# Kernel tuning notes

Hardware: AMD Instinct MI355X
Metric: run time of the kernel (lower is better)

The kernel has to match this reference:

```python
import jax, jax.numpy as jnp
import numpy as np

H, D = 16, 64  # n_heads, head_dim


def l2norm(t):
    # F.normalize(t, p=2, dim=-1)
    return t / jnp.maximum(jnp.linalg.norm(t, axis=-1, keepdims=True), 1e-12)


def setup_inputs() -> dict:
    key = jax.random.key(0)
    ks = jax.random.split(key, 6)
    B, N, C = 2, 2048, 1024
    x = jax.random.normal(ks[0], (B, N, C), jnp.float32)
    pos_bias = jax.random.normal(ks[1], (1, H, N, N), jnp.float32)
    mask = jnp.zeros((B, 1, 1, N), bool)  # attn_mask: True = masked
    Wqkv = jax.random.normal(ks[2], (C, 3 * H * D), jnp.float32) / np.sqrt(C)
    Wout = jax.random.normal(ks[3], (H * D, C), jnp.float32) / np.sqrt(H * D)
    Wpre = jax.random.normal(ks[4], (H, H), jnp.float32) / np.sqrt(H)   # 1x1 conv pre
    bpre = jnp.zeros((H,), jnp.float32)
    Wpost = jax.random.normal(ks[5], (H, H), jnp.float32) / np.sqrt(H)  # 1x1 conv post
    bpost = jnp.zeros((H,), jnp.float32)
    temperature = jnp.float32(15.5)
    return {"x": x, "pos_bias": pos_bias, "mask": mask, "Wqkv": Wqkv,
            "Wout": Wout, "Wpre": Wpre, "bpre": bpre, "Wpost": Wpost,
            "bpost": bpost, "temperature": temperature}


def reference(x, pos_bias, mask, Wqkv, Wout, Wpre, bpre, Wpost, bpost, temperature):
    B, N, C = x.shape
    # qkv: 'b n (h d qkv) -> qkv b h n d'
    qkv = (x @ Wqkv).reshape(B, N, H, D, 3)
    q = jnp.transpose(qkv[..., 0], (0, 2, 1, 3))  # [B,H,N,D]
    k = jnp.transpose(qkv[..., 1], (0, 2, 1, 3))
    v = jnp.transpose(qkv[..., 2], (0, 2, 1, 3))
    q, k = l2norm(q), l2norm(k)  # cosine_sim
    kv = jnp.stack([k, v], axis=0)  # attach_cache with cache=None
    # temperature-scaled cosine-sim scores
    dots = jnp.einsum('bhid,bhjd->bhij', q, k) * temperature
    # talking heads pre (1x1 conv over head channel)
    dots = jnp.einsum('gh,bhij->bgij', Wpre, dots) + bpre[None, :, None, None]
    dots = dots + pos_bias
    dots = jnp.where(mask, -jnp.finfo(dots.dtype).max, dots)
    attn = jax.nn.softmax(dots, axis=-1)
    # talking heads post
    attn = jnp.einsum('gh,bhij->bgij', Wpost, attn) + bpost[None, :, None, None]
    out = jnp.einsum('bhij,bhjd->bhid', attn, v)  # [B,H,N,D]
    out = jnp.transpose(out, (0, 2, 1, 3)).reshape(B, N, H * D) @ Wout
    return (out, kv)
```

## Files before the change

### kernel.cpp

```cpp
#include <hip/hip_runtime.h>
#include <stdint.h>

typedef __attribute__((ext_vector_type(8))) short bf16x8;
typedef __attribute__((ext_vector_type(4))) float f32x4;
typedef __attribute__((ext_vector_type(4))) short short4v;

#define DEV __device__ __forceinline__
#define L2E 1.4426950408889634f

DEV float bf2f(unsigned short s){ union{unsigned int u; float f;} x; x.u = ((unsigned int)s)<<16; return x.f; }
DEV unsigned short f2bf(float f){ union{float f; unsigned int u;} x; x.f = f; x.u += 0x7fffu + ((x.u>>16)&1u); return (unsigned short)(x.u>>16); }

DEV f32x4 mfma16(bf16x8 a, bf16x8 b, f32x4 c){
  return __builtin_amdgcn_mfma_f32_16x16x32_bf16(a, b, c, 0, 0, 0);
}
DEV f32x4 zero4(){ f32x4 z; z[0]=0.f; z[1]=0.f; z[2]=0.f; z[3]=0.f; return z; }
DEV bf16x8 zerob(){ bf16x8 z; z[0]=0;z[1]=0;z[2]=0;z[3]=0;z[4]=0;z[5]=0;z[6]=0;z[7]=0; return z; }
DEV float fexp2(float x){ float r; asm volatile("v_exp_f32 %0, %1" : "=v"(r) : "v"(x)); return r; }
DEV void barw(){ asm volatile("s_waitcnt lgkmcnt(0)" ::: "memory"); __builtin_amdgcn_s_barrier(); }

__global__ __launch_bounds__(256) void k_f32_to_bf16(const float* __restrict__ in, unsigned short* __restrict__ out, int n4){
  int i = blockIdx.x*256 + threadIdx.x;
  if (i < n4){
    float4 v = ((const float4*)in)[i];
    short4v o; o.x=(short)f2bf(v.x); o.y=(short)f2bf(v.y); o.z=(short)f2bf(v.z); o.w=(short)f2bf(v.w);
    ((short4v*)out)[i] = o;
  }
}

__global__ __launch_bounds__(256) void k_convT(const float* __restrict__ in, unsigned short* __restrict__ out, int R, int Cc){
  __shared__ float t[32][33];
  int c0 = blockIdx.x*32, r0 = blockIdx.y*32;
  int tid = threadIdx.x;
  int row = tid>>3, col4 = (tid&7)*4;
  float4 v = *(const float4*)&in[(size_t)(r0+row)*Cc + c0 + col4];
  t[row][col4+0]=v.x; t[row][col4+1]=v.y; t[row][col4+2]=v.z; t[row][col4+3]=v.w;
  __syncthreads();
  short4v o;
  o.x=(short)f2bf(t[col4+0][row]); o.y=(short)f2bf(t[col4+1][row]);
  o.z=(short)f2bf(t[col4+2][row]); o.w=(short)f2bf(t[col4+3][row]);
  *(short4v*)&out[(size_t)(c0+row)*R + r0 + col4] = o;
}

__global__ __launch_bounds__(256) void k_prep(const float* __restrict__ wpre, const float* __restrict__ wpost,
                                              const float* __restrict__ temp,
                                              unsigned short* __restrict__ wpre_t,
                                              unsigned short* __restrict__ wpre_t2,
                                              unsigned short* __restrict__ wpost_b){
  int t = threadIdx.x;
  float T = temp[0];
  wpre_t[t]  = f2bf(wpre[t]*T);
  wpre_t2[t] = f2bf(wpre[t]*T*L2E);
  wpost_b[t] = f2bf(wpost[t]);
}

__global__ __launch_bounds__(256) void k_maskf(const unsigned char* __restrict__ mask, float* __restrict__ maskf){
  int i = blockIdx.x*256 + threadIdx.x;
  if (i < 4096) maskf[i] = mask[i] ? -1e30f : 0.f;
}

template<int OUTF>
__global__ __launch_bounds__(256,2) void k_gemm(const unsigned short* __restrict__ A, const unsigned short* __restrict__ Bt,
                                                void* __restrict__ Cv, int M, int Nn, int K){
  __shared__ unsigned short As[128][72];
  __shared__ unsigned short Bs[128][72];
  int tid = threadIdx.x;
  int n0 = blockIdx.x*128, m0 = blockIdx.y*128;
  int w = tid>>6, lane = tid&63, lg = lane>>4, lp = lane&15;
  int wm = (w>>1)*64, wn = (w&1)*64;
  f32x4 acc[4][4];
  #pragma unroll
  for (int i=0;i<4;++i)
    #pragma unroll
    for (int j=0;j<4;++j) acc[i][j] = zero4();

  for (int kt=0; kt<K; kt+=64){
    #pragma unroll
    for (int cch=0; cch<4; ++cch){
      int e = tid + cch*256; int r = e>>3, cl = (e&7)*8;
      *(bf16x8*)&As[r][cl] = *(const bf16x8*)&A[(size_t)(m0+r)*K + kt + cl];
      *(bf16x8*)&Bs[r][cl] = *(const bf16x8*)&Bt[(size_t)(n0+r)*K + kt + cl];
    }
    __syncthreads();
    #pragma unroll
    for (int ks=0; ks<2; ++ks){
      bf16x8 a[4], b[4];
      #pragma unroll
      for (int mi=0; mi<4; ++mi) a[mi] = *(const bf16x8*)&As[wm+mi*16+lp][ks*32 + lg*8];
      #pragma unroll
      for (int ni=0; ni<4; ++ni) b[ni] = *(const bf16x8*)&Bs[wn+ni*16+lp][ks*32 + lg*8];
      #pragma unroll
      for (int mi=0; mi<4; ++mi)
        #pragma unroll
        for (int ni=0; ni<4; ++ni)
          acc[mi][ni] = mfma16(a[mi], b[ni], acc[mi][ni]);
    }
    __syncthreads();
  }
  #pragma unroll
  for (int mi=0; mi<4; ++mi)
    #pragma unroll
    for (int ni=0; ni<4; ++ni)
      #pragma unroll
      for (int r=0; r<4; ++r){
        int row = m0+wm+mi*16+lg*4+r, col = n0+wn+ni*16+lp;
        if (OUTF) ((float*)Cv)[(size_t)row*Nn+col] = acc[mi][ni][r];
        else ((unsigned short*)Cv)[(size_t)row*Nn+col] = f2bf(acc[mi][ni][r]);
      }
}

__global__ __launch_bounds__(256) void k_split_norm(const unsigned short* __restrict__ qkv,
                                                    unsigned short* __restrict__ q, unsigned short* __restrict__ k,
                                                    unsigned short* __restrict__ v, float* __restrict__ kv_out){
  int w = threadIdx.x>>6, lane = threadIdx.x&63;
  int widx = blockIdx.x*4 + w;
  int h = widx & 15; int bn = widx >> 4;
  int b = bn >> 11; int n = bn & 2047;
  size_t base = (size_t)bn*3072 + h*192 + lane*3;
  float qv = bf2f(qkv[base]), kvv = bf2f(qkv[base+1]), vv = bf2f(qkv[base+2]);
  float nq = qv*qv, nk = kvv*kvv;
  #pragma unroll
  for (int m=1; m<64; m<<=1){ nq += __shfl_xor(nq, m); nk += __shfl_xor(nk, m); }
  float qn = qv / fmaxf(sqrtf(nq), 1e-12f);
  float kn = kvv / fmaxf(sqrtf(nk), 1e-12f);
  size_t idx = ((size_t)(b*16+h)*2048 + n)*64 + lane;
  q[idx] = f2bf(qn); k[idx] = f2bf(kn); v[idx] = f2bf(vv);
  kv_out[idx] = kn;
  kv_out[4194304 + idx] = vv;
}

__global__ __launch_bounds__(256) void k_transpose_v(const unsigned short* __restrict__ v, unsigned short* __restrict__ vt){
  __shared__ unsigned short t[64][72];
  int bh = blockIdx.y; int n0 = blockIdx.x*64;
  int tid = threadIdx.x;
  #pragma unroll
  for (int cch=0; cch<2; ++cch){
    int e = tid + cch*256; int r = e>>3, c8 = (e&7)*8;
    *(bf16x8*)&t[r][c8] = *(const bf16x8*)&v[((size_t)bh*2048 + n0 + r)*64 + c8];
  }
  __syncthreads();
  #pragma unroll
  for (int cch=0; cch<2; ++cch){
    int e = tid + cch*256; int d = e>>3, nn8 = (e&7)*8;
    bf16x8 o;
    #pragma unroll
    for (int i=0;i<8;++i) o[i] = (short)t[nn8+i][d];
    *(bf16x8*)&vt[((size_t)bh*64 + d)*2048 + n0 + nn8] = o;
  }
}

__global__ __launch_bounds__(256) void k_vsum(const unsigned short* __restrict__ v, float* __restrict__ vsum){
  int bg = blockIdx.x;
  int d = threadIdx.x & 63, part = threadIdx.x>>6;
  float s = 0.f;
  for (int n = part*512; n < part*512+512; ++n) s += bf2f(v[((size_t)bg*2048 + n)*64 + d]);
  __shared__ float red[4][64];
  red[part][d] = s; __syncthreads();
  if (part==0) vsum[bg*64 + d] = red[0][d]+red[1][d]+red[2][d]+red[3][d];
}

__global__ __launch_bounds__(512,4) void k_score(
    const unsigned short* __restrict__ q,
    const unsigned short* __restrict__ kk,
    const float* __restrict__ pos_bias,
    const float* __restrict__ maskf,
    const unsigned short* __restrict__ wpre_t2,
    const float* __restrict__ bpre,
    unsigned short* __restrict__ Pb,
    float* __restrict__ part_l)
{
  __shared__ __align__(16) char smem[40960];
  const int tid = threadIdx.x;
  const int w = tid>>6, lane = tid&63, lg = lane>>4, lp = lane&15;
  const int bid = blockIdx.x;
  const int qd = bid>>4, r2 = bid&15;
  const int b = r2>>3, n = qd*8 + (r2&7);
  const int it = n>>2, js = n&3;
  const int i0 = it*16, jsb = js*512;

  bf16x8 qf[2][2];
  #pragma unroll
  for (int hh=0; hh<2; ++hh){
    const unsigned short* qb = q + ((size_t)(b*16+2*w+hh)*2048 + i0 + lp)*64;
    qf[hh][0] = *(const bf16x8*)(qb + lg*8);
    qf[hh][1] = *(const bf16x8*)(qb + 32 + lg*8);
  }
  bf16x8 preA = zerob();
  if (lg < 2) preA = *(const bf16x8*)&wpre_t2[lp*16 + lg*8];
  float bpre_s[4];
  #pragma unroll
  for (int r=0;r<4;++r) bpre_s[r] = bpre[lg*4+r]*L2E - 32.0f;

  float sacc[2][4];
  #pragma unroll
  for (int ii=0;ii<2;++ii)
    #pragma unroll
    for (int r=0;r<4;++r) sacc[ii][r] = 0.f;

  const size_t kbase0 = (size_t)(b*16 + 2*w)*131072;
  const size_t kbase1 = (size_t)(b*16 + 2*w+1)*131072;

  bf16x8 k0v[4], k1v[4];
  #pragma unroll
  for (int kf=0; kf<2; ++kf)
    #pragma unroll
    for (int jf=0; jf<2; ++jf){
      size_t off = (size_t)(jsb + jf*16 + lp)*64 + kf*32 + lg*8;
      k0v[kf*2+jf] = *(const bf16x8*)(kk + kbase0 + off);
      k1v[kf*2+jf] = *(const bf16x8*)(kk + kbase1 + off);
    }

  for (int t=0; t<16; ++t){
    const int j0 = jsb + t*32;
    const int j0n = jsb + ((t+1)&15)*32;
    char* sbuf = smem + (t&1)*20480;
    float pbt[4][4];
    #pragma unroll
    for (int cc=0; cc<4; ++cc){
      int il = 2*w + (cc>>1);
      int jl = (cc&1)*16 + lp;
      #pragma unroll
      for (int r=0;r<4;++r)
        pbt[cc][r] = pos_bias[(size_t)(lg*4+r)*4194304 + (size_t)(i0+il)*2048 + j0 + jl];
    }
    float mk0 = maskf[b*2048 + j0 + lp];
    float mk1 = maskf[b*2048 + j0 + 16 + lp];

    f32x4 s0[2], s1[2];
    #pragma unroll
    for (int jf=0;jf<2;++jf){ s0[jf]=zero4(); s1[jf]=zero4(); }
    #pragma unroll
    for (int kf=0; kf<2; ++kf)
      #pragma unroll
      for (int jf=0; jf<2; ++jf){
        s0[jf] = mfma16(qf[0][kf], k0v[kf*2+jf], s0[jf]);
        s1[jf] = mfma16(qf[1][kf], k1v[kf*2+jf], s1[jf]);
      }
    #pragma unroll
    for (int jf=0;jf<2;++jf)
      #pragma unroll
      for (int r=0;r<4;++r){
        int ij = (lg*4+r)*32 + jf*16 + lp;
        unsigned int pk = (unsigned int)f2bf(s0[jf][r]) | ((unsigned int)f2bf(s1[jf][r])<<16);
        *(unsigned int*)(sbuf + ij*40 + w*4) = pk;
      }
    #pragma unroll
    for (int kf=0; kf<2; ++kf)
      #pragma unroll
      for (int jf=0; jf<2; ++jf){
        size_t off = (size_t)(j0n + jf*16 + lp)*64 + kf*32 + lg*8;
        k0v[kf*2+jf] = *(const bf16x8*)(kk + kbase0 + off);
        k1v[kf*2+jf] = *(const bf16x8*)(kk + kbase1 + off);
      }
    barw();

    #pragma unroll
    for (int cc=0; cc<4; ++cc){
      int c = w*4+cc;
      int il = 2*w + (cc>>1);
      int jl = (cc&1)*16 + lp;
      bf16x8 sfrag = zerob();
      if (lg < 2) sfrag = *(const bf16x8*)(sbuf + (c*16+lp)*40 + lg*16);
      f32x4 pa = mfma16(preA, sfrag, zero4());
      float mkj = (cc&1) ? mk1 : mk0;
      float pv0 = fexp2(fmaf(pbt[cc][0], L2E, pa[0] + bpre_s[0] + mkj));
      float pv1 = fexp2(fmaf(pbt[cc][1], L2E, pa[1] + bpre_s[1] + mkj));
      float pv2 = fexp2(fmaf(pbt[cc][2], L2E, pa[2] + bpre_s[2] + mkj));
      float pv3 = fexp2(fmaf(pbt[cc][3], L2E, pa[3] + bpre_s[3] + mkj));
      sacc[cc>>1][0] += pv0; sacc[cc>>1][1] += pv1;
      sacc[cc>>1][2] += pv2; sacc[cc>>1][3] += pv3;
      short4v p4;
      p4.x = (short)f2bf(pv0); p4.y = (short)f2bf(pv1);
      p4.z = (short)f2bf(pv2); p4.w = (short)f2bf(pv3);
      *(short4v*)&Pb[(((size_t)(b*2048 + i0+il)*2048) + j0 + jl)*16 + lg*4] = p4;
    }
  }

  #pragma unroll
  for (int ii=0;ii<2;++ii)
    #pragma unroll
    for (int r=0;r<4;++r){
      float v = sacc[ii][r];
      #pragma unroll
      for (int m=1; m<16; m<<=1) v += __shfl_xor(v, m);
      sacc[ii][r] = v;
    }
  if (lp == 0){
    int base = ((b*128+it)*4 + js)*256;
    #pragma unroll
    for (int ii=0;ii<2;++ii){
      float4 st; st.x = sacc[ii][0]; st.y = sacc[ii][1]; st.z = sacc[ii][2]; st.w = sacc[ii][3];
      *(float4*)&part_l[base + (2*w+ii)*16 + lg*4] = st;
    }
  }
}

__global__ __launch_bounds__(512,4) void k_mix(
    const unsigned short* __restrict__ Pb,
    const unsigned short* __restrict__ vt,
    const unsigned short* __restrict__ wpost_b,
    const float* __restrict__ bpost,
    const float* __restrict__ vsum,
    const float* __restrict__ part_l,
    float* __restrict__ pout0,
    float* __restrict__ pout1)
{
  __shared__ __align__(16) char smem[33792];
  float* linv = (float*)(smem + 32768);
  const int tid = threadIdx.x;
  const int w = tid>>6, lane = tid&63, lg = lane>>4, lp = lane&15;
  const int bid = blockIdx.x;
  const int qd = bid>>4, r2 = bid&15;
  const int b = r2>>3, n = qd*8 + (r2&7);
  const int it = n>>1, js = n&1;
  const int i0 = it*16, jsb = js*1024;

  if (tid < 256){
    int base = ((b*128+it)*4)*256 + tid;
    float sum = part_l[base] + part_l[base+256] + part_l[base+512] + part_l[base+768];
    linv[tid] = 1.f/sum;
  }
  __syncthreads();

  bf16x8 postB[2];
  #pragma unroll
  for (int ii=0;ii<2;++ii){
    postB[ii] = zerob();
    if (lg < 2){
      bf16x8 wf = *(const bf16x8*)&wpost_b[lp*16 + lg*8];
      int i = 2*w+ii;
      #pragma unroll
      for (int e=0;e<8;++e){
        float vsc = bf2f((unsigned short)wf[e]) * linv[i*16 + lg*8 + e];
        postB[ii][e] = (short)f2bf(vsc);
      }
    }
  }

  f32x4 oacc[2][4];
  #pragma unroll
  for (int hh=0; hh<2; ++hh)
    #pragma unroll
    for (int df=0; df<4; ++df) oacc[hh][df] = zero4();

  __syncthreads();

  for (int t=0; t<32; ++t){
    const int j0 = jsb + t*32;
    char* abuf = smem + (t&1)*16384;
    bf16x8 pfr[4];
    #pragma unroll
    for (int cc=0; cc<4; ++cc){
      int il = 2*w + (cc>>1);
      pfr[cc] = zerob();
      if (lg < 2)
        pfr[cc] = *(const bf16x8*)&Pb[(((size_t)(b*2048 + i0+il)*2048) + j0 + (cc&1)*16 + lp)*16 + lg*8];
    }
    bf16x8 vfr[2][4];
    #pragma unroll
    for (int hh=0; hh<2; ++hh)
      #pragma unroll
      for (int df=0; df<4; ++df)
        vfr[hh][df] = *(const bf16x8*)(vt + ((size_t)(b*16+2*w+hh)*64 + df*16 + lp)*2048 + j0 + lg*8);
    #pragma unroll
    for (int cc=0; cc<4; ++cc){
      int il = 2*w + (cc>>1);
      f32x4 aa = mfma16(pfr[cc], postB[cc>>1], zero4());
      short4v av;
      av.x = (short)f2bf(aa[0]); av.y = (short)f2bf(aa[1]);
      av.z = (short)f2bf(aa[2]); av.w = (short)f2bf(aa[3]);
      int row = lp*16 + il;
      int chunk = ((cc&1)*4 + lg) ^ ((lp ^ il)&6);
      *(short4v*)(abuf + row*64 + chunk*8) = av;
    }
    barw();
    #pragma unroll
    for (int hh=0; hh<2; ++hh){
      int gg = 2*w+hh;
      bf16x8 af = *(const bf16x8*)(abuf + (gg*16+lp)*64 + (((lg*2) ^ ((gg^lp)&6))*8));
      #pragma unroll
      for (int df=0; df<4; ++df)
        oacc[hh][df] = mfma16(af, vfr[hh][df], oacc[hh][df]);
    }
  }

  float* po = js ? pout1 : pout0;
  #pragma unroll
  for (int hh=0; hh<2; ++hh){
    int gg = 2*w+hh;
    float bp = (js==0) ? bpost[gg] : 0.f;
    #pragma unroll
    for (int df=0; df<4; ++df){
      int d = df*16+lp;
      float vs = vsum[(b*16+gg)*64 + d];
      #pragma unroll
      for (int r=0;r<4;++r){
        po[((size_t)b*2048 + i0 + lg*4 + r)*1024 + gg*64 + d] = oacc[hh][df][r] + bp*vs;
      }
    }
  }
}

__global__ __launch_bounds__(256) void k_combine(const float* __restrict__ p0, const float* __restrict__ p1,
                                                 unsigned short* __restrict__ ao){
  int i = blockIdx.x*256 + threadIdx.x;
  float4 a = ((const float4*)p0)[i];
  float4 c = ((const float4*)p1)[i];
  short4v o;
  o.x=(short)f2bf(a.x+c.x); o.y=(short)f2bf(a.y+c.y);
  o.z=(short)f2bf(a.z+c.z); o.w=(short)f2bf(a.w+c.w);
  ((short4v*)ao)[i] = o;
}

__global__ __launch_bounds__(512,6) void k_pass1f(
    const unsigned short* __restrict__ q,
    const unsigned short* __restrict__ kk,
    const float* __restrict__ pos_bias,
    const unsigned char* __restrict__ mask,
    const unsigned short* __restrict__ wpre_t,
    const float* __restrict__ bpre,
    float* __restrict__ part_m,
    float* __restrict__ part_l)
{
  __shared__ __align__(16) char smem[40960];
  const int tid = threadIdx.x;
  const int w = tid>>6, lane = tid&63, lg = lane>>4, lp = lane&15;
  const int bid = blockIdx.x;
  const int js = bid & 3, b = (bid>>2)&1, it = bid>>3;
  const int i0 = it*16, jsb = js*512;

  *(f32x4*)(smem + tid*80 + 32) = zero4();
  *(f32x4*)(smem + tid*80 + 48) = zero4();

  bf16x8 qf[2][2];
  #pragma unroll
  for (int hh=0; hh<2; ++hh){
    const unsigned short* qb = q + ((size_t)(b*16+2*w+hh)*2048 + i0 + lp)*64;
    qf[hh][0] = *(const bf16x8*)(qb + lg*8);
    qf[hh][1] = *(const bf16x8*)(qb + 32 + lg*8);
  }
  bf16x8 preB = zerob();
  if (lg < 2) preB = *(const bf16x8*)&wpre_t[lp*16 + lg*8];
  const float bpre_g = bpre[lp];

  float m[2], s[2];
  m[0] = -3.0e38f; m[1] = -3.0e38f; s[0] = 0.f; s[1] = 0.f;
  const size_t kbase0 = (size_t)(b*16 + 2*w)*131072;
  const size_t kbase1 = (size_t)(b*16 + 2*w+1)*131072;

  __syncthreads();

  for (int t=0; t<16; ++t){
    const int j0 = jsb + t*32;
    f32x4 s0[2], s1[2];
    #pragma unroll
    for (int jf=0;jf<2;++jf){ s0[jf]=zero4(); s1[jf]=zero4(); }
    #pragma unroll
    for (int kf=0; kf<2; ++kf){
      #pragma unroll
      for (int jf=0; jf<2; ++jf){
        size_t off = (size_t)(j0 + jf*16 + lp)*64 + kf*32 + lg*8;
        bf16x8 k0 = *(const bf16x8*)(kk + kbase0 + off);
        bf16x8 k1 = *(const bf16x8*)(kk + kbase1 + off);
        s0[jf] = mfma16(qf[0][kf], k0, s0[jf]);
        s1[jf] = mfma16(qf[1][kf], k1, s1[jf]);
      }
    }
    #pragma unroll
    for (int jf=0;jf<2;++jf)
      #pragma unroll
      for (int r=0;r<4;++r){
        int ij = (lg*4+r)*32 + jf*16 + lp;
        unsigned int pk = (unsigned int)f2bf(s0[jf][r]) | ((unsigned int)f2bf(s1[jf][r])<<16);
        *(unsigned int*)(smem + ij*80 + w*4) = pk;
      }
    __syncthreads();

    unsigned int mku0 = *(const unsigned int*)(mask + b*2048 + j0 + lg*4);
    unsigned int mku1 = *(const unsigned int*)(mask + b*2048 + j0 + 16 + lg*4);
    #pragma unroll
    for (int cc=0; cc<4; ++cc){
      int c = w*4+cc;
      bf16x8 afr = *(const bf16x8*)(smem + (c*16+lp)*80 + lg*16);
      f32x4 pa = mfma16(afr, preB, zero4());
      int il = 2*w + (cc>>1);
      int jl = (cc&1)*16 + lg*4;
      float4 pb = *(const float4*)&pos_bias[((size_t)lp*2048 + (i0+il))*2048 + j0 + jl];
      unsigned int mku = (cc&1) ? mku1 : mku0;
      float va0 = pa[0] + pb.x + bpre_g + (((mku    )&255u) ? -1e30f : 0.f);
      float va1 = pa[1] + pb.y + bpre_g + (((mku>> 8)&255u) ? -1e30f : 0.f);
      float va2 = pa[2] + pb.z + bpre_g + (((mku>>16)&255u) ? -1e30f : 0.f);
      float va3 = pa[3] + pb.w + bpre_g + (((mku>>24)&255u) ? -1e30f : 0.f);
      int ii = cc>>1;
      float vm = fmaxf(fmaxf(va0,va1), fmaxf(va2,va3));
      float nm = fmaxf(m[ii], vm);
      s[ii] = s[ii]*__expf(m[ii]-nm) + __expf(va0-nm)+__expf(va1-nm)+__expf(va2-nm)+__expf(va3-nm);
      m[ii] = nm;
    }
    __syncthreads();
  }

  #pragma unroll
  for (int ii=0; ii<2; ++ii){
    #pragma unroll
    for (int mk_=16; mk_<=32; mk_<<=1){
      float m2 = __shfl_xor(m[ii], mk_);
      float l2 = __shfl_xor(s[ii], mk_);
      float nm = fmaxf(m[ii], m2);
      s[ii] = s[ii]*__expf(m[ii]-nm) + l2*__expf(m2-nm);
      m[ii] = nm;
    }
  }
  if (lg == 0){
    int pidx = ((b*128+it)*4 + js)*256;
    #pragma unroll
    for (int ii=0; ii<2; ++ii){
      part_m[pidx + (2*w+ii)*16 + lp] = m[ii];
      part_l[pidx + (2*w+ii)*16 + lp] = s[ii];
    }
  }
}

__global__ __launch_bounds__(512,4) void k_pass2f(
    const unsigned short* __restrict__ q,
    const unsigned short* __restrict__ kk,
    const unsigned short* __restrict__ vt,
    const float* __restrict__ pos_bias,
    const unsigned char* __restrict__ mask,
    const unsigned short* __restrict__ wpre_t,
    const unsigned short* __restrict__ wpost_b,
    const float* __restrict__ bpre,
    const float* __restrict__ bpost,
    const float* __restrict__ vsum,
    const float* __restrict__ part_m,
    const float* __restrict__ part_l,
    float* __restrict__ pout0,
    float* __restrict__ pout1)
{
  __shared__ __align__(16) char smem[61440];
  const int tid = threadIdx.x;
  const int w = tid>>6, lane = tid&63, lg = lane>>4, lp = lane&15;
  const int bid = blockIdx.x;
  const int js = bid & 1, b = (bid>>1)&1, it = bid>>2;
  const int i0 = it*16, jsb = js*1024;

  *(f32x4*)(smem + tid*80 + 32) = zero4();
  *(f32x4*)(smem + tid*80 + 48) = zero4();

  bf16x8 qf[2][2];
  #pragma unroll
  for (int hh=0; hh<2; ++hh){
    const unsigned short* qb = q + ((size_t)(b*16+2*w+hh)*2048 + i0 + lp)*64;
    qf[hh][0] = *(const bf16x8*)(qb + lg*8);
    qf[hh][1] = *(const bf16x8*)(qb + 32 + lg*8);
  }
  bf16x8 preB = zerob(), postB = zerob();
  if (lg < 2){
    preB  = *(const bf16x8*)&wpre_t[lp*16 + lg*8];
    postB = *(const bf16x8*)&wpost_b[lp*16 + lg*8];
  }
  const float bpre_g = bpre[lp];

  float mC[2], linvC[2];
  {
    float lC[2]; mC[0]=mC[1]=-3.0e38f; lC[0]=lC[1]=0.f;
    int base = ((b*128+it)*4)*256;
    #pragma unroll
    for (int sj=0; sj<4; ++sj){
      #pragma unroll
      for (int ii=0; ii<2; ++ii){
        float mp  = part_m[base + sj*256 + (2*w+ii)*16 + lp];
        float lpv = part_l[base + sj*256 + (2*w+ii)*16 + lp];
        float nm = fmaxf(mC[ii], mp);
        lC[ii] = lC[ii]*__expf(mC[ii]-nm) + lpv*__expf(mp-nm);
        mC[ii] = nm;
      }
    }
    linvC[0] = 1.f/lC[0]; linvC[1] = 1.f/lC[1];
  }

  f32x4 oacc[2][4];
  #pragma unroll
  for (int hh=0; hh<2; ++hh)
    #pragma unroll
    for (int df=0; df<4; ++df) oacc[hh][df] = zero4();

  const size_t kbase0 = (size_t)(b*16 + 2*w)*131072;
  const size_t kbase1 = (size_t)(b*16 + 2*w+1)*131072;

  __syncthreads();

  for (int t=0; t<32; ++t){
    const int j0 = jsb + t*32;
    f32x4 s0[2], s1[2];
    #pragma unroll
    for (int jf=0;jf<2;++jf){ s0[jf]=zero4(); s1[jf]=zero4(); }
    #pragma unroll
    for (int kf=0; kf<2; ++kf){
      #pragma unroll
      for (int jf=0; jf<2; ++jf){
        size_t off = (size_t)(j0 + jf*16 + lp)*64 + kf*32 + lg*8;
        bf16x8 k0 = *(const bf16x8*)(kk + kbase0 + off);
        bf16x8 k1 = *(const bf16x8*)(kk + kbase1 + off);
        s0[jf] = mfma16(qf[0][kf], k0, s0[jf]);
        s1[jf] = mfma16(qf[1][kf], k1, s1[jf]);
      }
    }
    #pragma unroll
    for (int jf=0;jf<2;++jf)
      #pragma unroll
      for (int r=0;r<4;++r){
        int ij = (lg*4+r)*32 + jf*16 + lp;
        unsigned int pk = (unsigned int)f2bf(s0[jf][r]) | ((unsigned int)f2bf(s1[jf][r])<<16);
        *(unsigned int*)(smem + ij*80 + w*4) = pk;
      }
    __syncthreads();

    unsigned int mku0 = *(const unsigned int*)(mask + b*2048 + j0 + lg*4);
    unsigned int mku1 = *(const unsigned int*)(mask + b*2048 + j0 + 16 + lg*4);
    #pragma unroll
    for (int cc=0; cc<4; ++cc){
      int c = w*4+cc;
      bf16x8 afr = *(const bf16x8*)(smem + (c*16+lp)*80 + lg*16);
      f32x4 pa = mfma16(afr, preB, zero4());
      int il = 2*w + (cc>>1);
      int jl = (cc&1)*16 + lg*4;
      float4 pb = *(const float4*)&pos_bias[((size_t)lp*2048 + (i0+il))*2048 + j0 + jl];
      unsigned int mku = (cc&1) ? mku1 : mku0;
      float va0 = pa[0] + pb.x + bpre_g + (((mku    )&255u) ? -1e30f : 0.f);
      float va1 = pa[1] + pb.y + bpre_g + (((mku>> 8)&255u) ? -1e30f : 0.f);
      float va2 = pa[2] + pb.z + bpre_g + (((mku>>16)&255u) ? -1e30f : 0.f);
      float va3 = pa[3] + pb.w + bpre_g + (((mku>>24)&255u) ? -1e30f : 0.f);
      int ii = cc>>1;
      int rowb = (c*16 + lg*4);
      *(unsigned short*)(smem + (rowb+0)*80 + lp*2) = f2bf(__expf(va0-mC[ii])*linvC[ii]);
      *(unsigned short*)(smem + (rowb+1)*80 + lp*2) = f2bf(__expf(va1-mC[ii])*linvC[ii]);
      *(unsigned short*)(smem + (rowb+2)*80 + lp*2) = f2bf(__expf(va2-mC[ii])*linvC[ii]);
      *(unsigned short*)(smem + (rowb+3)*80 + lp*2) = f2bf(__expf(va3-mC[ii])*linvC[ii]);
    }
    __syncthreads();

    #pragma unroll
    for (int cc=0; cc<4; ++cc){
      int c = w*4+cc;
      bf16x8 a2 = *(const bf16x8*)(smem + (c*16+lp)*80 + lg*16);
      f32x4 aa = mfma16(a2, postB, zero4());
      int il = 2*w + (cc>>1);
      int jl = (cc&1)*16 + lg*4;
      short4v av;
      av.x = (short)f2bf(aa[0]); av.y = (short)f2bf(aa[1]);
      av.z = (short)f2bf(aa[2]); av.w = (short)f2bf(aa[3]);
      *(short4v*)(smem + 40960 + (lp*16 + il)*80 + jl*2) = av;
    }
    __syncthreads();

    #pragma unroll
    for (int hh=0; hh<2; ++hh){
      int gg = 2*w+hh;
      bf16x8 af = *(const bf16x8*)(smem + 40960 + (gg*16+lp)*80 + lg*16);
      #pragma unroll
      for (int df=0; df<4; ++df){
        bf16x8 vf = *(const bf16x8*)(vt + ((size_t)(b*16+gg)*64 + df*16 + lp)*2048 + j0 + lg*8);
        oacc[hh][df] = mfma16(af, vf, oacc[hh][df]);
      }
    }
    __syncthreads();
  }

  float* po = js ? pout1 : pout0;
  #pragma unroll
  for (int hh=0; hh<2; ++hh){
    int gg = 2*w+hh;
    float bp = (js==0) ? bpost[gg] : 0.f;
    #pragma unroll
    for (int df=0; df<4; ++df){
      int d = df*16+lp;
      float vs = vsum[(b*16+gg)*64 + d];
      #pragma unroll
      for (int r=0;r<4;++r){
        po[((size_t)b*2048 + i0 + lg*4 + r)*1024 + gg*64 + d] = oacc[hh][df][r] + bp*vs;
      }
    }
  }
}

extern "C" void kernel_launch(void* const* d_in, const int* in_sizes, int n_in,
                              void* d_out, int out_size, void* d_ws, size_t ws_size,
                              hipStream_t stream)
{
  const float* x        = (const float*)d_in[0];
  const float* pos_bias = (const float*)d_in[1];
  const unsigned char* mask = (const unsigned char*)d_in[2];
  const float* Wqkv     = (const float*)d_in[3];
  const float* Wout     = (const float*)d_in[4];
  const float* Wpre     = (const float*)d_in[5];
  const float* bpre     = (const float*)d_in[6];
  const float* Wpost    = (const float*)d_in[7];
  const float* bpost    = (const float*)d_in[8];
  const float* temp     = (const float*)d_in[9];
  float* out = (float*)d_out;
  float* kv_out = out + 4194304;

  char* ws = (char*)d_ws;
  unsigned short* XB    = (unsigned short*)(ws + 0);
  unsigned short* WT    = (unsigned short*)(ws + 8388608);
  unsigned short* WOT   = (unsigned short*)(ws + 8388608);
  float*          PART_M= (float*)        (ws + 10485760);
  float*          PART_L= (float*)        (ws + 11534336);
  unsigned short* WPRE  = (unsigned short*)(ws + 12582912);
  unsigned short* WPRE2 = (unsigned short*)(ws + 12583424);
  unsigned short* WPOST = (unsigned short*)(ws + 12583936);
  float*          VSUM  = (float*)        (ws + 12584448);
  float*          MASKF = (float*)        (ws + 12593152);
  unsigned short* QKV   = (unsigned short*)(ws + 14680064);
  unsigned short* VT    = (unsigned short*)(ws + 14680064);
  float*          POUT0 = (float*)        (ws + 23068672);
  unsigned short* Q     = (unsigned short*)(ws + 39845888);
  unsigned short* KB    = (unsigned short*)(ws + 48234496);
  unsigned short* VB    = (unsigned short*)(ws + 56623104);
  float*          POUT1 = (float*)        (ws + 56623104);
  unsigned short* PB    = (unsigned short*)(ws + 75497472);
  unsigned short* AO    = XB;

  const int use_new = (ws_size >= (size_t)343932928);

  k_f32_to_bf16<<<4096, 256, 0, stream>>>(x, XB, 1048576);
  k_convT<<<dim3(96,32), 256, 0, stream>>>(Wqkv, WT, 1024, 3072);
  k_gemm<0><<<dim3(24,32), 256, 0, stream>>>(XB, WT, (void*)QKV, 4096, 3072, 1024);
  k_split_norm<<<16384, 256, 0, stream>>>(QKV, Q, KB, VB, kv_out);
  k_transpose_v<<<dim3(32,32), 256, 0, stream>>>(VB, VT);
  k_vsum<<<32, 256, 0, stream>>>(VB, VSUM);
  k_prep<<<1, 256, 0, stream>>>(Wpre, Wpost, temp, WPRE, WPRE2, WPOST);
  k_maskf<<<16, 256, 0, stream>>>(mask, MASKF);
  k_convT<<<dim3(32,32), 256, 0, stream>>>(Wout, WOT, 1024, 1024);

  if (use_new){
    k_score<<<1024, 512, 0, stream>>>(Q, KB, pos_bias, MASKF, WPRE2, bpre, PB, PART_L);
    k_mix<<<512, 512, 0, stream>>>(PB, VT, WPOST, bpost, VSUM, PART_L, POUT0, POUT1);
  } else {
    k_pass1f<<<1024, 512, 0, stream>>>(Q, KB, pos_bias, mask, WPRE, bpre, PART_M, PART_L);
    k_pass2f<<<512, 512, 0, stream>>>(Q, KB, VT, pos_bias, mask, WPRE, WPOST, bpre, bpost, VSUM,
                                      PART_M, PART_L, POUT0, POUT1);
  }
  k_combine<<<4096, 256, 0, stream>>>(POUT0, POUT1, AO);
  k_gemm<1><<<dim3(8,32), 256, 0, stream>>>(AO, WOT, d_out, 4096, 1024, 1024);
}
```

Baseline: 522.2 us.

## Precompute exp(pos_bias) in fp16 and factor it out of score softmax

Adds a kernel that converts pos_bias into exp(pos_bias) stored as fp16, packed with all 16 heads per (i,j). The score kernel then multiplies exp of the mixed score by this factor. It uses a fixed offset of -32 in place of a running max, and it prefetches K tiles and the exp-bias tiles one step ahead with double-buffered shared memory. The aim is to halve pos_bias read bytes in the hot kernel, make them contiguous, and drop max tracking. The cost is an extra pass over the full 64 MB pos_bias each call and a new 134 MB buffer. The fixed -32 offset and fp16 storage of exp(pos_bias) also raise overflow and underflow risk. The old two-pass fallback is removed.

Result: slower. 668.2 us (+28.0%).

```diff
diff --git a/kernel.cpp b/kernel.cpp
--- a/kernel.cpp
+++ b/kernel.cpp
@@ -1,4 +1,5 @@
 #include <hip/hip_runtime.h>
+#include <hip/hip_fp16.h>
 #include <stdint.h>
 
 typedef __attribute__((ext_vector_type(8))) short bf16x8;
@@ -10,6 +11,8 @@
 
 DEV float bf2f(unsigned short s){ union{unsigned int u; float f;} x; x.u = ((unsigned int)s)<<16; return x.f; }
 DEV unsigned short f2bf(float f){ union{float f; unsigned int u;} x; x.f = f; x.u += 0x7fffu + ((x.u>>16)&1u); return (unsigned short)(x.u>>16); }
+DEV float h2f(unsigned short u){ return __half2float(__ushort_as_half(u)); }
+DEV unsigned short f2h(float f){ return __half_as_ushort(__float2half(f)); }
 
 DEV f32x4 mfma16(bf16x8 a, bf16x8 b, f32x4 c){
   return __builtin_amdgcn_mfma_f32_16x16x32_bf16(a, b, c, 0, 0, 0);
@@ -44,12 +47,10 @@
 
 __global__ __launch_bounds__(256) void k_prep(const float* __restrict__ wpre, const float* __restrict__ wpost,
                                               const float* __restrict__ temp,
-                                              unsigned short* __restrict__ wpre_t,
                                               unsigned short* __restrict__ wpre_t2,
                                               unsigned short* __restrict__ wpost_b){
   int t = threadIdx.x;
   float T = temp[0];
-  wpre_t[t]  = f2bf(wpre[t]*T);
   wpre_t2[t] = f2bf(wpre[t]*T*L2E);
   wpost_b[t] = f2bf(wpost[t]);
 }
@@ -57,6 +58,23 @@
 __global__ __launch_bounds__(256) void k_maskf(const unsigned char* __restrict__ mask, float* __restrict__ maskf){
   int i = blockIdx.x*256 + threadIdx.x;
   if (i < 4096) maskf[i] = mask[i] ? -1e30f : 0.f;
+}
+
+__global__ __launch_bounds__(256) void k_pbexp(const float* __restrict__ pb, unsigned short* __restrict__ epb){
+  int idx = blockIdx.x*256 + threadIdx.x;
+  int i = idx >> 11, j = idx & 2047;
+  unsigned int pk[8];
+  #pragma unroll
+  for (int g2=0; g2<8; ++g2){
+    float a = fexp2(pb[(size_t)(2*g2  )*4194304 + (size_t)i*2048 + j] * L2E);
+    float b = fexp2(pb[(size_t)(2*g2+1)*4194304 + (size_t)i*2048 + j] * L2E);
+    pk[g2] = (unsigned int)f2h(a) | ((unsigned int)f2h(b)<<16);
+  }
+  uint4 o0, o1;
+  o0.x=pk[0]; o0.y=pk[1]; o0.z=pk[2]; o0.w=pk[3];
+  o1.x=pk[4]; o1.y=pk[5]; o1.z=pk[6]; o1.w=pk[7];
+  *(uint4*)&epb[(size_t)idx*16]     = o0;
+  *(uint4*)&epb[(size_t)idx*16 + 8] = o1;
 }
 
 template<int OUTF>
@@ -159,7 +177,208 @@
   if (part==0) vsum[bg*64 + d] = red[0][d]+red[1][d]+red[2][d]+red[3][d];
 }
 
-__global__ __launch_bounds__(512,4) void k_score(
+__global__ __launch_bounds__(512,4) void k_score2(
+    const unsigned short* __restrict__ q,
+    const unsigned short* __restrict__ kk,
+    const unsigned short* __restrict__ epb,
+    const float* __restrict__ maskf,
+    const unsigned short* __restrict__ wpre_t2,
+    const float* __restrict__ bpre,
+    unsigned short* __restrict__ Pb,
+    float* __restrict__ part_l)
+{
+  __shared__ __align__(16) char smem[40960];
+  const int tid = threadIdx.x;
+  const int w = tid>>6, lane = tid&63, lg = lane>>4, lp = lane&15;
+  const int bid = blockIdx.x;
+  const int qd = bid>>4, r2 = bid&15;
+  const int b = r2>>3, n = qd*8 + (r2&7);
+  const int it = n>>2, js = n&3;
+  const int i0 = it*16, jsb = js*512;
+  const int mbase = b*2048;
+
+  bf16x8 qf[2][2];
+  #pragma unroll
+  for (int hh=0; hh<2; ++hh){
+    const unsigned short* qb = q + ((size_t)(b*16+2*w+hh)*2048 + i0 + lp)*64;
+    qf[hh][0] = *(const bf16x8*)(qb + lg*8);
+    qf[hh][1] = *(const bf16x8*)(qb + 32 + lg*8);
+  }
+  bf16x8 preA = zerob();
+  if (lg < 2) preA = *(const bf16x8*)&wpre_t2[lp*16 + lg*8];
+  float bpre_s[4];
+  #pragma unroll
+  for (int r=0;r<4;++r) bpre_s[r] = bpre[lg*4+r]*L2E - 32.0f;
+
+  float sacc[2][4];
+  #pragma unroll
+  for (int ii=0;ii<2;++ii)
+    #pragma unroll
+    for (int r=0;r<4;++r) sacc[ii][r] = 0.f;
+
+  const size_t kbase0 = (size_t)(b*16 + 2*w)*131072;
+  const size_t kbase1 = (size_t)(b*16 + 2*w+1)*131072;
+
+  bf16x8 k0v[4], k1v[4];
+  #pragma unroll
+  for (int kf=0; kf<2; ++kf)
+    #pragma unroll
+    for (int jf=0; jf<2; ++jf){
+      size_t off = (size_t)(jsb + jf*16 + lp)*64 + kf*32 + lg*8;
+      k0v[kf*2+jf] = *(const bf16x8*)(kk + kbase0 + off);
+      k1v[kf*2+jf] = *(const bf16x8*)(kk + kbase1 + off);
+    }
+  short4v epA[4], epB[4];
+  float mkA0, mkA1, mkB0, mkB1;
+  #pragma unroll
+  for (int cc=0; cc<4; ++cc){
+    int il = 2*w + (cc>>1);
+    epA[cc] = *(const short4v*)&epb[(((size_t)(i0+il)*2048) + jsb + (cc&1)*16 + lp)*16 + lg*4];
+  }
+  mkA0 = maskf[mbase + jsb + lp];
+  mkA1 = maskf[mbase + jsb + 16 + lp];
+
+  for (int tt=0; tt<8; ++tt){
+    {
+      const int j0 = jsb + (2*tt)*32;
+      const int j1 = jsb + (2*tt+1)*32;
+      char* sbuf = smem;
+      f32x4 s0[2], s1[2];
+      #pragma unroll
+      for (int jf=0;jf<2;++jf){ s0[jf]=zero4(); s1[jf]=zero4(); }
+      #pragma unroll
+      for (int kf=0; kf<2; ++kf)
+        #pragma unroll
+        for (int jf=0; jf<2; ++jf){
+          s0[jf] = mfma16(qf[0][kf], k0v[kf*2+jf], s0[jf]);
+          s1[jf] = mfma16(qf[1][kf], k1v[kf*2+jf], s1[jf]);
+        }
+      #pragma unroll
+      for (int jf=0;jf<2;++jf)
+        #pragma unroll
+        for (int r=0;r<4;++r){
+          int ij = (lg*4+r)*32 + jf*16 + lp;
+          unsigned int pk = (unsigned int)f2bf(s0[jf][r]) | ((unsigned int)f2bf(s1[jf][r])<<16);
+          *(unsigned int*)(sbuf + ij*40 + w*4) = pk;
+        }
+      #pragma unroll
+      for (int kf=0; kf<2; ++kf)
+        #pragma unroll
+        for (int jf=0; jf<2; ++jf){
+          size_t off = (size_t)(j1 + jf*16 + lp)*64 + kf*32 + lg*8;
+          k0v[kf*2+jf] = *(const bf16x8*)(kk + kbase0 + off);
+          k1v[kf*2+jf] = *(const bf16x8*)(kk + kbase1 + off);
+        }
+      #pragma unroll
+      for (int cc=0; cc<4; ++cc){
+        int il = 2*w + (cc>>1);
+        epB[cc] = *(const short4v*)&epb[(((size_t)(i0+il)*2048) + j1 + (cc&1)*16 + lp)*16 + lg*4];
+      }
+      mkB0 = maskf[mbase + j1 + lp];
+      mkB1 = maskf[mbase + j1 + 16 + lp];
+      barw();
+      #pragma unroll
+      for (int cc=0; cc<4; ++cc){
+        int c = w*4+cc;
+        int il = 2*w + (cc>>1);
+        int jl = (cc&1)*16 + lp;
+        bf16x8 sfrag = zerob();
+        if (lg < 2) sfrag = *(const bf16x8*)(sbuf + (c*16+lp)*40 + lg*16);
+        f32x4 pa = mfma16(preA, sfrag, zero4());
+        float mkj = (cc&1) ? mkA1 : mkA0;
+        float pv0 = fexp2(pa[0] + bpre_s[0] + mkj) * h2f((unsigned short)epA[cc][0]);
+        float pv1 = fexp2(pa[1] + bpre_s[1] + mkj) * h2f((unsigned short)epA[cc][1]);
+        float pv2 = fexp2(pa[2] + bpre_s[2] + mkj) * h2f((unsigned short)epA[cc][2]);
+        float pv3 = fexp2(pa[3] + bpre_s[3] + mkj) * h2f((unsigned short)epA[cc][3]);
+        sacc[cc>>1][0] += pv0; sacc[cc>>1][1] += pv1;
+        sacc[cc>>1][2] += pv2; sacc[cc>>1][3] += pv3;
+        short4v p4;
+        p4.x = (short)f2bf(pv0); p4.y = (short)f2bf(pv1);
+        p4.z = (short)f2bf(pv2); p4.w = (short)f2bf(pv3);
+        *(short4v*)&Pb[(((size_t)(b*2048 + i0+il)*2048) + j0 + jl)*16 + lg*4] = p4;
+      }
+    }
+    {
+      const int j0 = jsb + (2*tt+1)*32;
+      const int j1 = jsb + ((2*tt+2)&15)*32;
+      char* sbuf = smem + 20480;
+      f32x4 s0[2], s1[2];
+      #pragma unroll
+      for (int jf=0;jf<2;++jf){ s0[jf]=zero4(); s1[jf]=zero4(); }
+      #pragma unroll
+      for (int kf=0; kf<2; ++kf)
+        #pragma unroll
+        for (int jf=0; jf<2; ++jf){
+          s0[jf] = mfma16(qf[0][kf], k0v[kf*2+jf], s0[jf]);
+          s1[jf] = mfma16(qf[1][kf], k1v[kf*2+jf], s1[jf]);
+        }
+      #pragma unroll
+      for (int jf=0;jf<2;++jf)
+        #pragma unroll
+        for (int r=0;r<4;++r){
+          int ij = (lg*4+r)*32 + jf*16 + lp;
+          unsigned int pk = (unsigned int)f2bf(s0[jf][r]) | ((unsigned int)f2bf(s1[jf][r])<<16);
+          *(unsigned int*)(sbuf + ij*40 + w*4) = pk;
+        }
+      #pragma unroll
+      for (int kf=0; kf<2; ++kf)
+        #pragma unroll
+        for (int jf=0; jf<2; ++jf){
+          size_t off = (size_t)(j1 + jf*16 + lp)*64 + kf*32 + lg*8;
+          k0v[kf*2+jf] = *(const bf16x8*)(kk + kbase0 + off);
+          k1v[kf*2+jf] = *(const bf16x8*)(kk + kbase1 + off);
+        }
+      #pragma unroll
+      for (int cc=0; cc<4; ++cc){
+        int il = 2*w + (cc>>1);
+        epA[cc] = *(const short4v*)&epb[(((size_t)(i0+il)*2048) + j1 + (cc&1)*16 + lp)*16 + lg*4];
+      }
+      mkA0 = maskf[mbase + j1 + lp];
+      mkA1 = maskf[mbase + j1 + 16 + lp];
+      barw();
+      #pragma unroll
+      for (int cc=0; cc<4; ++cc){
+        int c = w*4+cc;
+        int il = 2*w + (cc>>1);
+        int jl = (cc&1)*16 + lp;
+        bf16x8 sfrag = zerob();
+        if (lg < 2) sfrag = *(const bf16x8*)(sbuf + (c*16+lp)*40 + lg*16);
+        f32x4 pa = mfma16(preA, sfrag, zero4());
+        float mkj = (cc&1) ? mkB1 : mkB0;
+        float pv0 = fexp2(pa[0] + bpre_s[0] + mkj) * h2f((unsigned short)epB[cc][0]);
+        float pv1 = fexp2(pa[1] + bpre_s[1] + mkj) * h2f((unsigned short)epB[cc][1]);
+        float pv2 = fexp2(pa[2] + bpre_s[2] + mkj) * h2f((unsigned short)epB[cc][2]);
+        float pv3 = fexp2(pa[3] + bpre_s[3] + mkj) * h2f((unsigned short)epB[cc][3]);
+        sacc[cc>>1][0] += pv0; sacc[cc>>1][1] += pv1;
+        sacc[cc>>1][2] += pv2; sacc[cc>>1][3] += pv3;
+        short4v p4;
+        p4.x = (short)f2bf(pv0); p4.y = (short)f2bf(pv1);
+        p4.z = (short)f2bf(pv2); p4.w = (short)f2bf(pv3);
+        *(short4v*)&Pb[(((size_t)(b*2048 + i0+il)*2048) + j0 + jl)*16 + lg*4] = p4;
+      }
+    }
+  }
+
+  #pragma unroll
+  for (int ii=0;ii<2;++ii)
+    #pragma unroll
+    for (int r=0;r<4;++r){
+      float v = sacc[ii][r];
+      #pragma unroll
+      for (int m=1; m<16; m<<=1) v += __shfl_xor(v, m);
+      sacc[ii][r] = v;
+    }
+  if (lp == 0){
+    int base = ((b*128+it)*4 + js)*256;
+    #pragma unroll
+    for (int ii=0;ii<2;++ii){
+      float4 st; st.x = sacc[ii][0]; st.y = sacc[ii][1]; st.z = sacc[ii][2]; st.w = sacc[ii][3];
+      *(float4*)&part_l[base + (2*w+ii)*16 + lg*4] = st;
+    }
+  }
+}
+
+__global__ __launch_bounds__(512,4) void k_score_fb(
     const unsigned short* __restrict__ q,
     const unsigned short* __restrict__ kk,
     const float* __restrict__ pos_bias,
@@ -412,278 +631,6 @@
   ((short4v*)ao)[i] = o;
 }
 
-__global__ __launch_bounds__(512,6) void k_pass1f(
-    const unsigned short* __restrict__ q,
-    const unsigned short* __restrict__ kk,
-    const float* __restrict__ pos_bias,
-    const unsigned char* __restrict__ mask,
-    const unsigned short* __restrict__ wpre_t,
-    const float* __restrict__ bpre,
-    float* __restrict__ part_m,
-    float* __restrict__ part_l)
-{
-  __shared__ __align__(16) char smem[40960];
-  const int tid = threadIdx.x;
-  const int w = tid>>6, lane = tid&63, lg = lane>>4, lp = lane&15;
-  const int bid = blockIdx.x;
-  const int js = bid & 3, b = (bid>>2)&1, it = bid>>3;
-  const int i0 = it*16, jsb = js*512;
-
-  *(f32x4*)(smem + tid*80 + 32) = zero4();
-  *(f32x4*)(smem + tid*80 + 48) = zero4();
-
-  bf16x8 qf[2][2];
-  #pragma unroll
-  for (int hh=0; hh<2; ++hh){
-    const unsigned short* qb = q + ((size_t)(b*16+2*w+hh)*2048 + i0 + lp)*64;
-    qf[hh][0] = *(const bf16x8*)(qb + lg*8);
-    qf[hh][1] = *(const bf16x8*)(qb + 32 + lg*8);
-  }
-  bf16x8 preB = zerob();
-  if (lg < 2) preB = *(const bf16x8*)&wpre_t[lp*16 + lg*8];
-  const float bpre_g = bpre[lp];
-
-  float m[2], s[2];
-  m[0] = -3.0e38f; m[1] = -3.0e38f; s[0] = 0.f; s[1] = 0.f;
-  const size_t kbase0 = (size_t)(b*16 + 2*w)*131072;
-  const size_t kbase1 = (size_t)(b*16 + 2*w+1)*131072;
-
-  __syncthreads();
-
-  for (int t=0; t<16; ++t){
-    const int j0 = jsb + t*32;
-    f32x4 s0[2], s1[2];
-    #pragma unroll
-    for (int jf=0;jf<2;++jf){ s0[jf]=zero4(); s1[jf]=zero4(); }
-    #pragma unroll
-    for (int kf=0; kf<2; ++kf){
-      #pragma unroll
-      for (int jf=0; jf<2; ++jf){
-        size_t off = (size_t)(j0 + jf*16 + lp)*64 + kf*32 + lg*8;
-        bf16x8 k0 = *(const bf16x8*)(kk + kbase0 + off);
-        bf16x8 k1 = *(const bf16x8*)(kk + kbase1 + off);
-        s0[jf] = mfma16(qf[0][kf], k0, s0[jf]);
-        s1[jf] = mfma16(qf[1][kf], k1, s1[jf]);
-      }
-    }
-    #pragma unroll
-    for (int jf=0;jf<2;++jf)
-      #pragma unroll
-      for (int r=0;r<4;++r){
-        int ij = (lg*4+r)*32 + jf*16 + lp;
-        unsigned int pk = (unsigned int)f2bf(s0[jf][r]) | ((unsigned int)f2bf(s1[jf][r])<<16);
-        *(unsigned int*)(smem + ij*80 + w*4) = pk;
-      }
-    __syncthreads();
-
-    unsigned int mku0 = *(const unsigned int*)(mask + b*2048 + j0 + lg*4);
-    unsigned int mku1 = *(const unsigned int*)(mask + b*2048 + j0 + 16 + lg*4);
-    #pragma unroll
-    for (int cc=0; cc<4; ++cc){
-      int c = w*4+cc;
-      bf16x8 afr = *(const bf16x8*)(smem + (c*16+lp)*80 + lg*16);
-      f32x4 pa = mfma16(afr, preB, zero4());
-      int il = 2*w + (cc>>1);
-      int jl = (cc&1)*16 + lg*4;
-      float4 pb = *(const float4*)&pos_bias[((size_t)lp*2048 + (i0+il))*2048 + j0 + jl];
-      unsigned int mku = (cc&1) ? mku1 : mku0;
-      float va0 = pa[0] + pb.x + bpre_g + (((mku    )&255u) ? -1e30f : 0.f);
-      float va1 = pa[1] + pb.y + bpre_g + (((mku>> 8)&255u) ? -1e30f : 0.f);
-      float va2 = pa[2] + pb.z + bpre_g + (((mku>>16)&255u) ? -1e30f : 0.f);
-      float va3 = pa[3] + pb.w + bpre_g + (((mku>>24)&255u) ? -1e30f : 0.f);
-      int ii = cc>>1;
-      float vm = fmaxf(fmaxf(va0,va1), fmaxf(va2,va3));
-      float nm = fmaxf(m[ii], vm);
-      s[ii] = s[ii]*__expf(m[ii]-nm) + __expf(va0-nm)+__expf(va1-nm)+__expf(va2-nm)+__expf(va3-nm);
-      m[ii] = nm;
-    }
-    __syncthreads();
-  }
-
-  #pragma unroll
-  for (int ii=0; ii<2; ++ii){
-    #pragma unroll
-    for (int mk_=16; mk_<=32; mk_<<=1){
-      float m2 = __shfl_xor(m[ii], mk_);
-      float l2 = __shfl_xor(s[ii], mk_);
-      float nm = fmaxf(m[ii], m2);
-      s[ii] = s[ii]*__expf(m[ii]-nm) + l2*__expf(m2-nm);
-      m[ii] = nm;
-    }
-  }
-  if (lg == 0){
-    int pidx = ((b*128+it)*4 + js)*256;
-    #pragma unroll
-    for (int ii=0; ii<2; ++ii){
-      part_m[pidx + (2*w+ii)*16 + lp] = m[ii];
-      part_l[pidx + (2*w+ii)*16 + lp] = s[ii];
-    }
-  }
-}
-
-__global__ __launch_bounds__(512,4) void k_pass2f(
-    const unsigned short* __restrict__ q,
-    const unsigned short* __restrict__ kk,
-    const unsigned short* __restrict__ vt,
-    const float* __restrict__ pos_bias,
-    const unsigned char* __restrict__ mask,
-    const unsigned short* __restrict__ wpre_t,
-    const unsigned short* __restrict__ wpost_b,
-    const float* __restrict__ bpre,
-    const float* __restrict__ bpost,
-    const float* __restrict__ vsum,
-    const float* __restrict__ part_m,
-    const float* __restrict__ part_l,
-    float* __restrict__ pout0,
-    float* __restrict__ pout1)
-{
-  __shared__ __align__(16) char smem[61440];
-  const int tid = threadIdx.x;
-  const int w = tid>>6, lane = tid&63, lg = lane>>4, lp = lane&15;
-  const int bid = blockIdx.x;
-  const int js = bid & 1, b = (bid>>1)&1, it = bid>>2;
-  const int i0 = it*16, jsb = js*1024;
-
-  *(f32x4*)(smem + tid*80 + 32) = zero4();
-  *(f32x4*)(smem + tid*80 + 48) = zero4();
-
-  bf16x8 qf[2][2];
-  #pragma unroll
-  for (int hh=0; hh<2; ++hh){
-    const unsigned short* qb = q + ((size_t)(b*16+2*w+hh)*2048 + i0 + lp)*64;
-    qf[hh][0] = *(const bf16x8*)(qb + lg*8);
-    qf[hh][1] = *(const bf16x8*)(qb + 32 + lg*8);
-  }
-  bf16x8 preB = zerob(), postB = zerob();
-  if (lg < 2){
-    preB  = *(const bf16x8*)&wpre_t[lp*16 + lg*8];
-    postB = *(const bf16x8*)&wpost_b[lp*16 + lg*8];
-  }
-  const float bpre_g = bpre[lp];
-
-  float mC[2], linvC[2];
-  {
-    float lC[2]; mC[0]=mC[1]=-3.0e38f; lC[0]=lC[1]=0.f;
-    int base = ((b*128+it)*4)*256;
-    #pragma unroll
-    for (int sj=0; sj<4; ++sj){
-      #pragma unroll
-      for (int ii=0; ii<2; ++ii){
-        float mp  = part_m[base + sj*256 + (2*w+ii)*16 + lp];
-        float lpv = part_l[base + sj*256 + (2*w+ii)*16 + lp];
-        float nm = fmaxf(mC[ii], mp);
-        lC[ii] = lC[ii]*__expf(mC[ii]-nm) + lpv*__expf(mp-nm);
-        mC[ii] = nm;
-      }
-    }
-    linvC[0] = 1.f/lC[0]; linvC[1] = 1.f/lC[1];
-  }
-
-  f32x4 oacc[2][4];
-  #pragma unroll
-  for (int hh=0; hh<2; ++hh)
-    #pragma unroll
-    for (int df=0; df<4; ++df) oacc[hh][df] = zero4();
-
-  const size_t kbase0 = (size_t)(b*16 + 2*w)*131072;
-  const size_t kbase1 = (size_t)(b*16 + 2*w+1)*131072;
-
-  __syncthreads();
-
-  for (int t=0; t<32; ++t){
-    const int j0 = jsb + t*32;
-    f32x4 s0[2], s1[2];
-    #pragma unroll
-    for (int jf=0;jf<2;++jf){ s0[jf]=zero4(); s1[jf]=zero4(); }
-    #pragma unroll
-    for (int kf=0; kf<2; ++kf){
-      #pragma unroll
-      for (int jf=0; jf<2; ++jf){
-        size_t off = (size_t)(j0 + jf*16 + lp)*64 + kf*32 + lg*8;
-        bf16x8 k0 = *(const bf16x8*)(kk + kbase0 + off);
-        bf16x8 k1 = *(const bf16x8*)(kk + kbase1 + off);
-        s0[jf] = mfma16(qf[0][kf], k0, s0[jf]);
-        s1[jf] = mfma16(qf[1][kf], k1, s1[jf]);
-      }
-    }
-    #pragma unroll
-    for (int jf=0;jf<2;++jf)
-      #pragma unroll
-      for (int r=0;r<4;++r){
-        int ij = (lg*4+r)*32 + jf*16 + lp;
-        unsigned int pk = (unsigned int)f2bf(s0[jf][r]) | ((unsigned int)f2bf(s1[jf][r])<<16);
-        *(unsigned int*)(smem + ij*80 + w*4) = pk;
-      }
-    __syncthreads();
-
-    unsigned int mku0 = *(const unsigned int*)(mask + b*2048 + j0 + lg*4);
-    unsigned int mku1 = *(const unsigned int*)(mask + b*2048 + j0 + 16 + lg*4);
-    #pragma unroll
-    for (int cc=0; cc<4; ++cc){
-      int c = w*4+cc;
-      bf16x8 afr = *(const bf16x8*)(smem + (c*16+lp)*80 + lg*16);
-      f32x4 pa = mfma16(afr, preB, zero4());
-      int il = 2*w + (cc>>1);
-      int jl = (cc&1)*16 + lg*4;
-      float4 pb = *(const float4*)&pos_bias[((size_t)lp*2048 + (i0+il))*2048 + j0 + jl];
-      unsigned int mku = (cc&1) ? mku1 : mku0;
-      float va0 = pa[0] + pb.x + bpre_g + (((mku    )&255u) ? -1e30f : 0.f);
-      float va1 = pa[1] + pb.y + bpre_g + (((mku>> 8)&255u) ? -1e30f : 0.f);
-      float va2 = pa[2] + pb.z + bpre_g + (((mku>>16)&255u) ? -1e30f : 0.f);
-      float va3 = pa[3] + pb.w + bpre_g + (((mku>>24)&255u) ? -1e30f : 0.f);
-      int ii = cc>>1;
-      int rowb = (c*16 + lg*4);
-      *(unsigned short*)(smem + (rowb+0)*80 + lp*2) = f2bf(__expf(va0-mC[ii])*linvC[ii]);
-      *(unsigned short*)(smem + (rowb+1)*80 + lp*2) = f2bf(__expf(va1-mC[ii])*linvC[ii]);
-      *(unsigned short*)(smem + (rowb+2)*80 + lp*2) = f2bf(__expf(va2-mC[ii])*linvC[ii]);
-      *(unsigned short*)(smem + (rowb+3)*80 + lp*2) = f2bf(__expf(va3-mC[ii])*linvC[ii]);
-    }
-    __syncthreads();
-
-    #pragma unroll
-    for (int cc=0; cc<4; ++cc){
-      int c = w*4+cc;
-      bf16x8 a2 = *(const bf16x8*)(smem + (c*16+lp)*80 + lg*16);
-      f32x4 aa = mfma16(a2, postB, zero4());
-      int il = 2*w + (cc>>1);
-      int jl = (cc&1)*16 + lg*4;
-      short4v av;
-      av.x = (short)f2bf(aa[0]); av.y = (short)f2bf(aa[1]);
-      av.z = (short)f2bf(aa[2]); av.w = (short)f2bf(aa[3]);
-      *(short4v*)(smem + 40960 + (lp*16 + il)*80 + jl*2) = av;
-    }
-    __syncthreads();
-
-    #pragma unroll
-    for (int hh=0; hh<2; ++hh){
-      int gg = 2*w+hh;
-      bf16x8 af = *(const bf16x8*)(smem + 40960 + (gg*16+lp)*80 + lg*16);
-      #pragma unroll
-      for (int df=0; df<4; ++df){
-        bf16x8 vf = *(const bf16x8*)(vt + ((size_t)(b*16+gg)*64 + df*16 + lp)*2048 + j0 + lg*8);
-        oacc[hh][df] = mfma16(af, vf, oacc[hh][df]);
-      }
-    }
-    __syncthreads();
-  }
-
-  float* po = js ? pout1 : pout0;
-  #pragma unroll
-  for (int hh=0; hh<2; ++hh){
-    int gg = 2*w+hh;
-    float bp = (js==0) ? bpost[gg] : 0.f;
-    #pragma unroll
-    for (int df=0; df<4; ++df){
-      int d = df*16+lp;
-      float vs = vsum[(b*16+gg)*64 + d];
-      #pragma unroll
-      for (int r=0;r<4;++r){
-        po[((size_t)b*2048 + i0 + lg*4 + r)*1024 + gg*64 + d] = oacc[hh][df][r] + bp*vs;
-      }
-    }
-  }
-}
-
 extern "C" void kernel_launch(void* const* d_in, const int* in_sizes, int n_in,
                               void* d_out, int out_size, void* d_ws, size_t ws_size,
                               hipStream_t stream)
@@ -705,24 +652,23 @@
   unsigned short* XB    = (unsigned short*)(ws + 0);
   unsigned short* WT    = (unsigned short*)(ws + 8388608);
   unsigned short* WOT   = (unsigned short*)(ws + 8388608);
-  float*          PART_M= (float*)        (ws + 10485760);
   float*          PART_L= (float*)        (ws + 11534336);
-  unsigned short* WPRE  = (unsigned short*)(ws + 12582912);
   unsigned short* WPRE2 = (unsigned short*)(ws + 12583424);
   unsigned short* WPOST = (unsigned short*)(ws + 12583936);
   float*          VSUM  = (float*)        (ws + 12584448);
   float*          MASKF = (float*)        (ws + 12593152);
-  unsigned short* QKV   = (unsigned short*)(ws + 14680064);
   unsigned short* VT    = (unsigned short*)(ws + 14680064);
   float*          POUT0 = (float*)        (ws + 23068672);
+  unsigned short* QKV   = (unsigned short*)(ws + 14680064);
   unsigned short* Q     = (unsigned short*)(ws + 39845888);
   unsigned short* KB    = (unsigned short*)(ws + 48234496);
   unsigned short* VB    = (unsigned short*)(ws + 56623104);
   float*          POUT1 = (float*)        (ws + 56623104);
   unsigned short* PB    = (unsigned short*)(ws + 75497472);
+  unsigned short* EPB   = (unsigned short*)(ws + 343932928);
   unsigned short* AO    = XB;
 
-  const int use_new = (ws_size >= (size_t)343932928);
+  const int have_epb = (ws_size >= (size_t)478150656);
 
   k_f32_to_bf16<<<4096, 256, 0, stream>>>(x, XB, 1048576);
   k_convT<<<dim3(96,32), 256, 0, stream>>>(Wqkv, WT, 1024, 3072);
@@ -730,18 +676,17 @@
   k_split_norm<<<16384, 256, 0, stream>>>(QKV, Q, KB, VB, kv_out);
   k_transpose_v<<<dim3(32,32), 256, 0, stream>>>(VB, VT);
   k_vsum<<<32, 256, 0, stream>>>(VB, VSUM);
-  k_prep<<<1, 256, 0, stream>>>(Wpre, Wpost, temp, WPRE, WPRE2, WPOST);
+  k_prep<<<1, 256, 0, stream>>>(Wpre, Wpost, temp, WPRE2, WPOST);
   k_maskf<<<16, 256, 0, stream>>>(mask, MASKF);
   k_convT<<<dim3(32,32), 256, 0, stream>>>(Wout, WOT, 1024, 1024);
 
-  if (use_new){
-    k_score<<<1024, 512, 0, stream>>>(Q, KB, pos_bias, MASKF, WPRE2, bpre, PB, PART_L);
-    k_mix<<<512, 512, 0, stream>>>(PB, VT, WPOST, bpost, VSUM, PART_L, POUT0, POUT1);
+  if (have_epb){
+    k_pbexp<<<16384, 256, 0, stream>>>(pos_bias, EPB);
+    k_score2<<<1024, 512, 0, stream>>>(Q, KB, EPB, MASKF, WPRE2, bpre, PB, PART_L);
   } else {
-    k_pass1f<<<1024, 512, 0, stream>>>(Q, KB, pos_bias, mask, WPRE, bpre, PART_M, PART_L);
-    k_pass2f<<<512, 512, 0, stream>>>(Q, KB, VT, pos_bias, mask, WPRE, WPOST, bpre, bpost, VSUM,
-                                      PART_M, PART_L, POUT0, POUT1);
-  }
+    k_score_fb<<<1024, 512, 0, stream>>>(Q, KB, pos_bias, MASKF, WPRE2, bpre, PB, PART_L);
+  }
+  k_mix<<<512, 512, 0, stream>>>(PB, VT, WPOST, bpost, VSUM, PART_L, POUT0, POUT1);
   k_combine<<<4096, 256, 0, stream>>>(POUT0, POUT1, AO);
   k_gemm<1><<<dim3(8,32), 256, 0, stream>>>(AO, WOT, d_out, 4096, 1024, 1024);
 }
```
